# Optimization experiments

Hardware: AMD Instinct MI355X
Metric: run time of the kernel (lower is better)

## Reference

```python
import jax, jax.numpy as jnp
import numpy as np

B_, N, C, NH, NW = 2048, 64, 512, 16, 64  # N == window_size

def setup_inputs() -> dict:
    key = jax.random.key(0)
    k0, k1, k2, k3 = jax.random.split(key, 4)
    std = 0.02
    return {
        "inputs": jax.random.normal(k0, (B_, N, C), jnp.float32),
        "mask": jnp.zeros((NW, N, N), jnp.float32),  # (0 / -inf) additive window mask
        "qkv_w": jax.random.normal(k1, (3 * C, C), jnp.float32) * std,
        "qkv_b": jnp.zeros((3 * C,), jnp.float32),
        "proj_w": jax.random.normal(k2, (C, C), jnp.float32) * std,
        "proj_b": jnp.zeros((C,), jnp.float32),
        "bias_table": jax.random.normal(k3, (2 * N - 1, NH), jnp.float32) * std,
    }

def reference(inputs, mask, qkv_w, qkv_b, proj_w, proj_b, bias_table):
    b, n, c = inputs.shape
    nh = bias_table.shape[1]
    hd = c // nh
    scale = hd ** -0.5
    # qkv projection -> (3, B_, nh, N, hd)
    qkv = (inputs @ qkv_w.T + qkv_b).reshape(b, n, 3, nh, hd).transpose(2, 0, 3, 1, 4)
    q, k, v = qkv[0] * scale, qkv[1], qkv[2]
    attn = jnp.einsum('bhqd,bhkd->bhqk', q, k)  # (B_, nh, N, N)
    # 1D relative position bias, gathered from table
    rel_idx = jnp.arange(n)[:, None] - jnp.arange(n)[None, :] + (n - 1)  # (N, N)
    rel_bias = bias_table[rel_idx]                 # (N, N, nh)
    attn = attn + rel_bias.transpose(2, 0, 1)[None]  # add (nh, N, N)
    # additive window mask
    nw = mask.shape[0]
    attn = attn.reshape(b // nw, nw, nh, n, n) + mask[None, :, None]
    attn = jax.nn.softmax(attn.reshape(b, nh, n, n), axis=-1)
    out = jnp.einsum('bhqk,bhkd->bqhd', attn, v).reshape(b, n, c)
    return out @ proj_w.T + proj_b
```

## Files before the change

### kernel.cpp

```cpp
#include <hip/hip_runtime.h>

typedef __bf16 bf16x8 __attribute__((ext_vector_type(8)));
typedef float f32x4 __attribute__((ext_vector_type(4)));

__device__ __forceinline__ unsigned short f2bf(float x) {
  union { float f; unsigned int u; } c; c.f = x;
  unsigned int r = c.u + 0x7FFFu + ((c.u >> 16) & 1u);
  return (unsigned short)(r >> 16);
}

__global__ __launch_bounds__(256) void f32_to_bf16_vec4(
    const float* __restrict__ in, unsigned short* __restrict__ out, int n4) {
  int i = blockIdx.x * blockDim.x + threadIdx.x;
  int stride = gridDim.x * blockDim.x;
  const float4* in4 = (const float4*)in;
  ushort4* out4 = (ushort4*)out;
  for (; i < n4; i += stride) {
    float4 f = in4[i];
    ushort4 u;
    u.x = f2bf(f.x); u.y = f2bf(f.y); u.z = f2bf(f.z); u.w = f2bf(f.w);
    out4[i] = u;
  }
}

__global__ __launch_bounds__(256) void build_bias_mask(
    const float* __restrict__ bias_table,
    const float* __restrict__ mask,
    float* __restrict__ M) {
  const int idx = blockIdx.x * 256 + threadIdx.x;
  const int k = idx & 63, q = (idx >> 6) & 63, h = (idx >> 12) & 15, w = idx >> 16;
  M[idx] = bias_table[(q - k + 63) * 16 + h] + mask[(w * 64 + q) * 64 + k];
}

#define GLOAD_LDS16(gp, lp)                                                          \
  __builtin_amdgcn_global_load_lds(                                                  \
      (const __attribute__((address_space(1))) unsigned int*)(uintptr_t)(gp),        \
      (__attribute__((address_space(3))) unsigned int*)(uintptr_t)(lp), 16, 0, 0)

template <int NBN, int EPI>
__global__ __launch_bounds__(512, 2) void gemm256(
    const unsigned short* __restrict__ A,
    const unsigned short* __restrict__ B,
    const float* __restrict__ bias,
    void* __restrict__ C0, void* __restrict__ C1, void* __restrict__ C2,
    int ldc) {
  constexpr int K = 512;
  constexpr int NT = K / 64;
  __shared__ __attribute__((aligned(128))) char lds[131072];

  const int t = threadIdx.x;
  const int lane = t & 63;
  const int wid = t >> 6;
  const int wr = wid >> 2, wc = wid & 3;
  const int lr = lane & 15, lg = lane >> 4;

  const int nwg = gridDim.x;
  const int cpx = nwg >> 3;
  const int wgid = (blockIdx.x & 7) * cpx + (blockIdx.x >> 3);
  const int bm = wgid / NBN, bn = wgid % NBN;
  const int m0 = bm * 256, n0 = bn * 256;

  const char* Ab = (const char*)(A + (size_t)m0 * K);
  const char* Bb = (const char*)(B + (size_t)n0 * K);

  const int r3 = t >> 3, ps = t & 7;

  unsigned aoff[2][2], adst[2][2], boff[2][2], bdst[2][2];
#pragma unroll
  for (int j = 0; j < 2; ++j)
#pragma unroll
    for (int i = 0; i < 2; ++i) {
      const int rowA = i * 128 + j * 64 + r3;
      aoff[j][i] = (unsigned)((rowA * K + ((ps ^ (rowA & 7)) << 3)) * 2);
      adst[j][i] = (unsigned)(rowA * 128 + ps * 16);
      const int rowB = i * 128 + ((r3 >> 5) << 6) + j * 32 + (r3 & 31);
      boff[j][i] = (unsigned)((rowB * K + ((ps ^ (rowB & 7)) << 3)) * 2);
      bdst[j][i] = (unsigned)(65536 + rowB * 128 + ps * 16);
    }

#define STAGE_A(j, tt, buf)                                                   \
  do {                                                                        \
    GLOAD_LDS16(Ab + aoff[j][0] + (tt)*128, lds + (buf)*32768 + adst[j][0]);  \
    GLOAD_LDS16(Ab + aoff[j][1] + (tt)*128, lds + (buf)*32768 + adst[j][1]);  \
  } while (0)
#define STAGE_B(j, tt, buf)                                                   \
  do {                                                                        \
    GLOAD_LDS16(Bb + boff[j][0] + (tt)*128, lds + (buf)*32768 + bdst[j][0]);  \
    GLOAD_LDS16(Bb + boff[j][1] + (tt)*128, lds + (buf)*32768 + bdst[j][1]);  \
  } while (0)

  unsigned abase[2], bbase[2];
#pragma unroll
  for (int kk = 0; kk < 2; ++kk) {
    abase[kk] = (unsigned)((wr * 128 + lr) * 128 + (((kk * 4 + lg) ^ (lr & 7)) << 4));
    bbase[kk] = (unsigned)(65536 + (wc * 64 + lr) * 128 + (((kk * 4 + lg) ^ (lr & 7)) << 4));
  }

  f32x4 acc[8][4];
#pragma unroll
  for (int i = 0; i < 8; ++i)
#pragma unroll
    for (int j = 0; j < 4; ++j) acc[i][j] = f32x4{0.f, 0.f, 0.f, 0.f};

#define BAR_IN()                                         \
  __builtin_amdgcn_s_barrier();                          \
  asm volatile("s_waitcnt lgkmcnt(0)" ::: "memory");     \
  __builtin_amdgcn_sched_barrier(0);                     \
  __builtin_amdgcn_s_setprio(1)
#define MFMA16(QM, NTLO)                                                            \
  _Pragma("unroll") for (int mt = 0; mt < 4; ++mt)                                  \
    _Pragma("unroll") for (int nt = 0; nt < 2; ++nt)                                \
      _Pragma("unroll") for (int kk = 0; kk < 2; ++kk)                              \
        acc[(QM)*4 + mt][(NTLO) + nt] = __builtin_amdgcn_mfma_f32_16x16x32_bf16(    \
            af[mt][kk], bfr[(NTLO) + nt][kk], acc[(QM)*4 + mt][(NTLO) + nt], 0, 0, 0)

  STAGE_A(0, 0, 0); STAGE_B(0, 0, 0); STAGE_B(1, 0, 0); STAGE_A(1, 0, 0);
  STAGE_A(0, 1, 1); STAGE_B(0, 1, 1);
  asm volatile("s_waitcnt vmcnt(8)" ::: "memory");
  __builtin_amdgcn_s_barrier();

#pragma unroll
  for (int tt = 0; tt < NT; ++tt) {
    const int buf = tt & 1;
    const int nb = buf ^ 1;
    bf16x8 af[4][2], bfr[4][2];
#pragma unroll
    for (int nt = 0; nt < 2; ++nt)
#pragma unroll
      for (int kk = 0; kk < 2; ++kk)
        bfr[nt][kk] = *(const bf16x8*)(lds + buf * 32768 + bbase[kk] + nt * 2048);
#pragma unroll
    for (int mt = 0; mt < 4; ++mt)
#pragma unroll
      for (int kk = 0; kk < 2; ++kk)
        af[mt][kk] = *(const bf16x8*)(lds + buf * 32768 + abase[kk] + mt * 2048);
    if (tt + 1 < NT) STAGE_B(1, tt + 1, nb);
    BAR_IN();
    MFMA16(0, 0);
    __builtin_amdgcn_s_setprio(0);
    if (tt == NT - 1) asm volatile("s_waitcnt vmcnt(2)" ::: "memory");
    else              asm volatile("s_waitcnt vmcnt(8)" ::: "memory");
    __builtin_amdgcn_s_barrier();
#pragma unroll
    for (int nt = 2; nt < 4; ++nt)
#pragma unroll
      for (int kk = 0; kk < 2; ++kk)
        bfr[nt][kk] = *(const bf16x8*)(lds + buf * 32768 + bbase[kk] + nt * 2048);
    if (tt + 1 < NT) STAGE_A(1, tt + 1, nb);
    BAR_IN();
    MFMA16(0, 2);
    __builtin_amdgcn_s_setprio(0);
    if (tt == NT - 1) asm volatile("s_waitcnt vmcnt(0)" ::: "memory");
    else              asm volatile("s_waitcnt vmcnt(8)" ::: "memory");
    __builtin_amdgcn_s_barrier();
#pragma unroll
    for (int mt = 0; mt < 4; ++mt)
#pragma unroll
      for (int kk = 0; kk < 2; ++kk)
        af[mt][kk] = *(const bf16x8*)(lds + buf * 32768 + abase[kk] + 8192 + mt * 2048);
    if (tt + 2 < NT) STAGE_A(0, tt + 2, buf);
    BAR_IN();
    MFMA16(1, 0);
    __builtin_amdgcn_s_setprio(0);
    if (tt < NT - 1) asm volatile("s_waitcnt vmcnt(8)" ::: "memory");
    __builtin_amdgcn_s_barrier();
    if (tt + 2 < NT) STAGE_B(0, tt + 2, buf);
    BAR_IN();
    MFMA16(1, 2);
    __builtin_amdgcn_s_setprio(0);
    if (tt < NT - 2)       asm volatile("s_waitcnt vmcnt(8)" ::: "memory");
    else if (tt == NT - 2) asm volatile("s_waitcnt vmcnt(4)" ::: "memory");
    __builtin_amdgcn_s_barrier();
  }
#undef MFMA16
#undef BAR_IN
#undef STAGE_A
#undef STAGE_B

#pragma unroll
  for (int qm = 0; qm < 2; ++qm)
#pragma unroll
    for (int mt = 0; mt < 4; ++mt)
#pragma unroll
      for (int nt = 0; nt < 4; ++nt) {
        const int n = n0 + wc * 64 + nt * 16 + lr;
        const float bv = bias[n];
        const f32x4 a4 = acc[qm * 4 + mt][nt];
        if constexpr (EPI == 2) {
          const int part = n >> 9;
          unsigned short* dst = part == 0 ? (unsigned short*)C0
                                 : (part == 1 ? (unsigned short*)C1 : (unsigned short*)C2);
          const float sc = (part == 0) ? 0.17677669529663687f : 1.0f;
          const int hh = (n >> 5) & 15, dd = n & 31;
#pragma unroll
          for (int r = 0; r < 4; ++r) {
            const int m = m0 + wr * 128 + qm * 64 + mt * 16 + lg * 4 + r;
            dst[((size_t)((m >> 6) * 16 + hh) * 64 + (m & 63)) * 32 + dd] =
                f2bf((a4[r] + bv) * sc);
          }
        } else {
#pragma unroll
          for (int r = 0; r < 4; ++r) {
            const int m = m0 + wr * 128 + qm * 64 + mt * 16 + lg * 4 + r;
            ((float*)C0)[(size_t)m * ldc + n] = a4[r] + bv;
          }
        }
      }
}

__global__ __launch_bounds__(128) void attn_kernel(
    const unsigned short* __restrict__ Qh,
    const unsigned short* __restrict__ Kh,
    const unsigned short* __restrict__ Vh,
    const float* __restrict__ M,
    unsigned short* __restrict__ attn_out
) {
  const int wv = threadIdx.x >> 6;
  const int bh = blockIdx.x * 2 + wv;
  const int b = bh >> 4, h = bh & 15;
  const int lane = threadIdx.x & 63;
  const int lr = lane & 15, lg = lane >> 4;

  __shared__ unsigned short VtS[2][32 * 72];
  __shared__ unsigned short PlS[2][16 * 72];
  unsigned short* Vt = VtS[wv];
  unsigned short* Pl = PlS[wv];

  const unsigned short* qb = Qh + (size_t)bh * 2048;
  const unsigned short* kb = Kh + (size_t)bh * 2048;
  const unsigned short* vg = Vh + (size_t)bh * 2048;

  bf16x8 vr[4];
#pragma unroll
  for (int i = 0; i < 4; ++i) vr[i] = ((const bf16x8*)(vg + lane * 32))[i];
  bf16x8 kf[4], qf[4];
#pragma unroll
  for (int nt = 0; nt < 4; ++nt)
    kf[nt] = *(const bf16x8*)(kb + (nt * 16 + lr) * 32 + lg * 8);
#pragma unroll
  for (int mt = 0; mt < 4; ++mt)
    qf[mt] = *(const bf16x8*)(qb + (mt * 16 + lr) * 32 + lg * 8);

  {
    __bf16* vt = (__bf16*)Vt;
#pragma unroll
    for (int d = 0; d < 8; ++d) {
      vt[(d)*72 + lane] = vr[0][d];
      vt[(d + 8) * 72 + lane] = vr[1][d];
      vt[(d + 16) * 72 + lane] = vr[2][d];
      vt[(d + 24) * 72 + lane] = vr[3][d];
    }
  }
  bf16x8 vfrag[2][2];
#pragma unroll
  for (int dt = 0; dt < 2; ++dt)
#pragma unroll
    for (int ki = 0; ki < 2; ++ki)
      vfrag[dt][ki] = *(const bf16x8*)(Vt + (dt * 16 + lr) * 72 + ki * 32 + lg * 8);

  const float* Mb = M + (size_t)((b & 63) * 16 + h) * 4096;

  f32x4 o[4][2];
#pragma unroll
  for (int i = 0; i < 4; ++i)
#pragma unroll
    for (int j = 0; j < 2; ++j) o[i][j] = f32x4{0.f, 0.f, 0.f, 0.f};
  float rinv[4][4];

#pragma unroll
  for (int mt = 0; mt < 4; ++mt) {
    float mv[4][4];
#pragma unroll
    for (int r = 0; r < 4; ++r)
#pragma unroll
      for (int nt = 0; nt < 4; ++nt)
        mv[r][nt] = Mb[(mt * 16 + lg * 4 + r) * 64 + nt * 16 + lr];

    f32x4 s[4];
#pragma unroll
    for (int nt = 0; nt < 4; ++nt) s[nt] = f32x4{0.f, 0.f, 0.f, 0.f};
    __builtin_amdgcn_s_setprio(1);
#pragma unroll
    for (int nt = 0; nt < 4; ++nt)
      s[nt] = __builtin_amdgcn_mfma_f32_16x16x32_bf16(qf[mt], kf[nt], s[nt], 0, 0, 0);
    __builtin_amdgcn_s_setprio(0);

#pragma unroll
    for (int r = 0; r < 4; ++r) {
      float v[4];
#pragma unroll
      for (int nt = 0; nt < 4; ++nt) v[nt] = s[nt][r] + mv[r][nt];
      float mx = fmaxf(fmaxf(v[0], v[1]), fmaxf(v[2], v[3]));
      mx = fmaxf(mx, __shfl_xor(mx, 1, 64));
      mx = fmaxf(mx, __shfl_xor(mx, 2, 64));
      mx = fmaxf(mx, __shfl_xor(mx, 4, 64));
      mx = fmaxf(mx, __shfl_xor(mx, 8, 64));
      float sum = 0.f;
#pragma unroll
      for (int nt = 0; nt < 4; ++nt) {
        v[nt] = __expf(v[nt] - mx);
        sum += v[nt];
      }
      sum += __shfl_xor(sum, 1, 64);
      sum += __shfl_xor(sum, 2, 64);
      sum += __shfl_xor(sum, 4, 64);
      sum += __shfl_xor(sum, 8, 64);
      rinv[mt][r] = __builtin_amdgcn_rcpf(sum);
#pragma unroll
      for (int nt = 0; nt < 4; ++nt)
        Pl[(lg * 4 + r) * 72 + nt * 16 + lr] = f2bf(v[nt]);
    }

    bf16x8 pa[2];
#pragma unroll
    for (int ki = 0; ki < 2; ++ki)
      pa[ki] = *(const bf16x8*)(Pl + lr * 72 + ki * 32 + lg * 8);
    __builtin_amdgcn_s_setprio(1);
#pragma unroll
    for (int dt = 0; dt < 2; ++dt)
#pragma unroll
      for (int ki = 0; ki < 2; ++ki)
        o[mt][dt] = __builtin_amdgcn_mfma_f32_16x16x32_bf16(pa[ki], vfrag[dt][ki], o[mt][dt], 0, 0, 0);
    __builtin_amdgcn_s_setprio(0);
  }

#pragma unroll
  for (int mt = 0; mt < 4; ++mt) {
#pragma unroll
    for (int r = 0; r < 4; ++r) {
      const int m = mt * 16 + lg * 4 + r;
      const float ri = rinv[mt][r];
#pragma unroll
      for (int dt = 0; dt < 2; ++dt) {
        const int d = dt * 16 + lr;
        attn_out[(size_t)(b * 64 + m) * 512 + h * 32 + d] = f2bf(o[mt][dt][r] * ri);
      }
    }
  }
}

extern "C" void kernel_launch(void* const* d_in, const int* in_sizes, int n_in,
                              void* d_out, int out_size, void* d_ws, size_t ws_size,
                              hipStream_t stream) {
  const float* X = (const float*)d_in[0];
  const float* mask = (const float*)d_in[1];
  const float* qkv_w = (const float*)d_in[2];
  const float* qkv_b = (const float*)d_in[3];
  const float* proj_w = (const float*)d_in[4];
  const float* proj_b = (const float*)d_in[5];
  const float* bias_table = (const float*)d_in[6];
  float* out = (float*)d_out;
  char* ws = (char*)d_ws;

  unsigned short* Xb      = (unsigned short*)(ws);
  unsigned short* Qh      = (unsigned short*)(ws + 134217728ull);
  unsigned short* Kh      = (unsigned short*)(ws + 268435456ull);
  unsigned short* Vh      = (unsigned short*)(ws + 402653184ull);
  unsigned short* attnout = (unsigned short*)(ws + 536870912ull);
  unsigned short* qkv_wb  = (unsigned short*)(ws + 671088640ull);
  unsigned short* proj_wb = (unsigned short*)(ws + 672661504ull);
  float*          Mf      = (float*)(ws + 673185792ull);

  f32_to_bf16_vec4<<<2048, 256, 0, stream>>>(X, Xb, 67108864 / 4);
  f32_to_bf16_vec4<<<768, 256, 0, stream>>>(qkv_w, qkv_wb, 786432 / 4);
  f32_to_bf16_vec4<<<256, 256, 0, stream>>>(proj_w, proj_wb, 262144 / 4);
  build_bias_mask<<<16384, 256, 0, stream>>>(bias_table, mask, Mf);

  gemm256<6, 2><<<3072, 512, 0, stream>>>(Xb, qkv_wb, qkv_b, (void*)Qh, (void*)Kh, (void*)Vh, 1536);

  attn_kernel<<<16384, 128, 0, stream>>>(Qh, Kh, Vh, Mf, attnout);

  gemm256<2, 0><<<1024, 512, 0, stream>>>(attnout, proj_wb, proj_b, (void*)out, nullptr, nullptr, 512);
}
```

Baseline: 577.5 us.

## Shrink GEMM tiles to 128x128 with simple double buffering; remap attention blocks

Replaces the 256x256, 8-wave GEMM with a 128x128, 4-wave GEMM that uses a plain double-buffered pipeline: the next K-slice is staged before the current one is computed, with a full vmcnt(0) wait each iteration. This quadruples the number of workgroups and halves LDS per block. The aim is better occupancy and tail balance, at the cost of less operand reuse per tile and a less overlapped schedule. The attention kernel also changes how blocks map to batch and head: each block now holds one head of two windows that are 64 batches apart, which changes how mask and bias rows are shared in cache.

Result: slower. 672.2 us (+16.4%).

```diff
diff --git a/kernel.cpp b/kernel.cpp
--- a/kernel.cpp
+++ b/kernel.cpp
@@ -38,7 +38,7 @@
       (__attribute__((address_space(3))) unsigned int*)(uintptr_t)(lp), 16, 0, 0)
 
 template <int NBN, int EPI>
-__global__ __launch_bounds__(512, 2) void gemm256(
+__global__ __launch_bounds__(256, 2) void gemm128(
     const unsigned short* __restrict__ A,
     const unsigned short* __restrict__ B,
     const float* __restrict__ bias,
@@ -46,166 +46,120 @@
     int ldc) {
   constexpr int K = 512;
   constexpr int NT = K / 64;
-  __shared__ __attribute__((aligned(128))) char lds[131072];
+  __shared__ __attribute__((aligned(128))) char lds[65536];
 
   const int t = threadIdx.x;
   const int lane = t & 63;
   const int wid = t >> 6;
-  const int wr = wid >> 2, wc = wid & 3;
+  const int wr = wid >> 1, wc = wid & 1;
   const int lr = lane & 15, lg = lane >> 4;
 
   const int nwg = gridDim.x;
   const int cpx = nwg >> 3;
   const int wgid = (blockIdx.x & 7) * cpx + (blockIdx.x >> 3);
   const int bm = wgid / NBN, bn = wgid % NBN;
-  const int m0 = bm * 256, n0 = bn * 256;
+  const int m0 = bm * 128, n0 = bn * 128;
 
   const char* Ab = (const char*)(A + (size_t)m0 * K);
   const char* Bb = (const char*)(B + (size_t)n0 * K);
 
   const int r3 = t >> 3, ps = t & 7;
 
-  unsigned aoff[2][2], adst[2][2], boff[2][2], bdst[2][2];
-#pragma unroll
-  for (int j = 0; j < 2; ++j)
-#pragma unroll
-    for (int i = 0; i < 2; ++i) {
-      const int rowA = i * 128 + j * 64 + r3;
-      aoff[j][i] = (unsigned)((rowA * K + ((ps ^ (rowA & 7)) << 3)) * 2);
-      adst[j][i] = (unsigned)(rowA * 128 + ps * 16);
-      const int rowB = i * 128 + ((r3 >> 5) << 6) + j * 32 + (r3 & 31);
-      boff[j][i] = (unsigned)((rowB * K + ((ps ^ (rowB & 7)) << 3)) * 2);
-      bdst[j][i] = (unsigned)(65536 + rowB * 128 + ps * 16);
-    }
-
-#define STAGE_A(j, tt, buf)                                                   \
-  do {                                                                        \
-    GLOAD_LDS16(Ab + aoff[j][0] + (tt)*128, lds + (buf)*32768 + adst[j][0]);  \
-    GLOAD_LDS16(Ab + aoff[j][1] + (tt)*128, lds + (buf)*32768 + adst[j][1]);  \
+  unsigned soff[4], adst[4], bdst[4];
+#pragma unroll
+  for (int i = 0; i < 4; ++i) {
+    const int row = i * 32 + r3;
+    soff[i] = (unsigned)((row * K + ((ps ^ (row & 7)) << 3)) * 2);
+    adst[i] = (unsigned)(row * 128 + ps * 16);
+    bdst[i] = (unsigned)(32768 + row * 128 + ps * 16);
+  }
+
+#define STAGE(tt, buf)                                                          \
+  do {                                                                          \
+    _Pragma("unroll") for (int i = 0; i < 4; ++i)                               \
+      GLOAD_LDS16(Ab + soff[i] + (tt)*128, lds + (buf)*16384 + adst[i]);        \
+    _Pragma("unroll") for (int i = 0; i < 4; ++i)                               \
+      GLOAD_LDS16(Bb + soff[i] + (tt)*128, lds + (buf)*16384 + bdst[i]);        \
   } while (0)
-#define STAGE_B(j, tt, buf)                                                   \
-  do {                                                                        \
-    GLOAD_LDS16(Bb + boff[j][0] + (tt)*128, lds + (buf)*32768 + bdst[j][0]);  \
-    GLOAD_LDS16(Bb + boff[j][1] + (tt)*128, lds + (buf)*32768 + bdst[j][1]);  \
-  } while (0)
 
   unsigned abase[2], bbase[2];
 #pragma unroll
   for (int kk = 0; kk < 2; ++kk) {
-    abase[kk] = (unsigned)((wr * 128 + lr) * 128 + (((kk * 4 + lg) ^ (lr & 7)) << 4));
-    bbase[kk] = (unsigned)(65536 + (wc * 64 + lr) * 128 + (((kk * 4 + lg) ^ (lr & 7)) << 4));
-  }
-
-  f32x4 acc[8][4];
-#pragma unroll
-  for (int i = 0; i < 8; ++i)
+    const unsigned swz = (unsigned)(((kk * 4 + lg) ^ (lr & 7)) << 4);
+    abase[kk] = (unsigned)((wr * 64 + lr) * 128) + swz;
+    bbase[kk] = (unsigned)(32768 + (wc * 64 + lr) * 128) + swz;
+  }
+
+  f32x4 acc[4][4];
+#pragma unroll
+  for (int i = 0; i < 4; ++i)
 #pragma unroll
     for (int j = 0; j < 4; ++j) acc[i][j] = f32x4{0.f, 0.f, 0.f, 0.f};
 
-#define BAR_IN()                                         \
-  __builtin_amdgcn_s_barrier();                          \
-  asm volatile("s_waitcnt lgkmcnt(0)" ::: "memory");     \
-  __builtin_amdgcn_sched_barrier(0);                     \
-  __builtin_amdgcn_s_setprio(1)
-#define MFMA16(QM, NTLO)                                                            \
-  _Pragma("unroll") for (int mt = 0; mt < 4; ++mt)                                  \
-    _Pragma("unroll") for (int nt = 0; nt < 2; ++nt)                                \
-      _Pragma("unroll") for (int kk = 0; kk < 2; ++kk)                              \
-        acc[(QM)*4 + mt][(NTLO) + nt] = __builtin_amdgcn_mfma_f32_16x16x32_bf16(    \
-            af[mt][kk], bfr[(NTLO) + nt][kk], acc[(QM)*4 + mt][(NTLO) + nt], 0, 0, 0)
-
-  STAGE_A(0, 0, 0); STAGE_B(0, 0, 0); STAGE_B(1, 0, 0); STAGE_A(1, 0, 0);
-  STAGE_A(0, 1, 1); STAGE_B(0, 1, 1);
-  asm volatile("s_waitcnt vmcnt(8)" ::: "memory");
+  STAGE(0, 0);
+  asm volatile("s_waitcnt vmcnt(0)" ::: "memory");
   __builtin_amdgcn_s_barrier();
 
 #pragma unroll
   for (int tt = 0; tt < NT; ++tt) {
     const int buf = tt & 1;
     const int nb = buf ^ 1;
+    if (tt + 1 < NT) STAGE(tt + 1, nb);
     bf16x8 af[4][2], bfr[4][2];
 #pragma unroll
-    for (int nt = 0; nt < 2; ++nt)
+    for (int mt = 0; mt < 4; ++mt)
 #pragma unroll
       for (int kk = 0; kk < 2; ++kk)
-        bfr[nt][kk] = *(const bf16x8*)(lds + buf * 32768 + bbase[kk] + nt * 2048);
+        af[mt][kk] = *(const bf16x8*)(lds + buf * 16384 + abase[kk] + mt * 2048);
+#pragma unroll
+    for (int nt = 0; nt < 4; ++nt)
+#pragma unroll
+      for (int kk = 0; kk < 2; ++kk)
+        bfr[nt][kk] = *(const bf16x8*)(lds + buf * 16384 + bbase[kk] + nt * 2048);
+    asm volatile("s_waitcnt lgkmcnt(0)" ::: "memory");
+    __builtin_amdgcn_sched_barrier(0);
+    __builtin_amdgcn_s_setprio(1);
 #pragma unroll
     for (int mt = 0; mt < 4; ++mt)
 #pragma unroll
-      for (int kk = 0; kk < 2; ++kk)
-        af[mt][kk] = *(const bf16x8*)(lds + buf * 32768 + abase[kk] + mt * 2048);
-    if (tt + 1 < NT) STAGE_B(1, tt + 1, nb);
-    BAR_IN();
-    MFMA16(0, 0);
+      for (int nt = 0; nt < 4; ++nt)
+#pragma unroll
+        for (int kk = 0; kk < 2; ++kk)
+          acc[mt][nt] = __builtin_amdgcn_mfma_f32_16x16x32_bf16(
+              af[mt][kk], bfr[nt][kk], acc[mt][nt], 0, 0, 0);
     __builtin_amdgcn_s_setprio(0);
-    if (tt == NT - 1) asm volatile("s_waitcnt vmcnt(2)" ::: "memory");
-    else              asm volatile("s_waitcnt vmcnt(8)" ::: "memory");
+    if (tt + 1 < NT) asm volatile("s_waitcnt vmcnt(0)" ::: "memory");
     __builtin_amdgcn_s_barrier();
-#pragma unroll
-    for (int nt = 2; nt < 4; ++nt)
-#pragma unroll
-      for (int kk = 0; kk < 2; ++kk)
-        bfr[nt][kk] = *(const bf16x8*)(lds + buf * 32768 + bbase[kk] + nt * 2048);
-    if (tt + 1 < NT) STAGE_A(1, tt + 1, nb);
-    BAR_IN();
-    MFMA16(0, 2);
-    __builtin_amdgcn_s_setprio(0);
-    if (tt == NT - 1) asm volatile("s_waitcnt vmcnt(0)" ::: "memory");
-    else              asm volatile("s_waitcnt vmcnt(8)" ::: "memory");
-    __builtin_amdgcn_s_barrier();
-#pragma unroll
-    for (int mt = 0; mt < 4; ++mt)
-#pragma unroll
-      for (int kk = 0; kk < 2; ++kk)
-        af[mt][kk] = *(const bf16x8*)(lds + buf * 32768 + abase[kk] + 8192 + mt * 2048);
-    if (tt + 2 < NT) STAGE_A(0, tt + 2, buf);
-    BAR_IN();
-    MFMA16(1, 0);
-    __builtin_amdgcn_s_setprio(0);
-    if (tt < NT - 1) asm volatile("s_waitcnt vmcnt(8)" ::: "memory");
-    __builtin_amdgcn_s_barrier();
-    if (tt + 2 < NT) STAGE_B(0, tt + 2, buf);
-    BAR_IN();
-    MFMA16(1, 2);
-    __builtin_amdgcn_s_setprio(0);
-    if (tt < NT - 2)       asm volatile("s_waitcnt vmcnt(8)" ::: "memory");
-    else if (tt == NT - 2) asm volatile("s_waitcnt vmcnt(4)" ::: "memory");
-    __builtin_amdgcn_s_barrier();
-  }
-#undef MFMA16
-#undef BAR_IN
-#undef STAGE_A
-#undef STAGE_B
-
-#pragma unroll
-  for (int qm = 0; qm < 2; ++qm)
-#pragma unroll
-    for (int mt = 0; mt < 4; ++mt)
-#pragma unroll
-      for (int nt = 0; nt < 4; ++nt) {
-        const int n = n0 + wc * 64 + nt * 16 + lr;
-        const float bv = bias[n];
-        const f32x4 a4 = acc[qm * 4 + mt][nt];
-        if constexpr (EPI == 2) {
-          const int part = n >> 9;
-          unsigned short* dst = part == 0 ? (unsigned short*)C0
-                                 : (part == 1 ? (unsigned short*)C1 : (unsigned short*)C2);
-          const float sc = (part == 0) ? 0.17677669529663687f : 1.0f;
-          const int hh = (n >> 5) & 15, dd = n & 31;
-#pragma unroll
-          for (int r = 0; r < 4; ++r) {
-            const int m = m0 + wr * 128 + qm * 64 + mt * 16 + lg * 4 + r;
-            dst[((size_t)((m >> 6) * 16 + hh) * 64 + (m & 63)) * 32 + dd] =
-                f2bf((a4[r] + bv) * sc);
-          }
-        } else {
-#pragma unroll
-          for (int r = 0; r < 4; ++r) {
-            const int m = m0 + wr * 128 + qm * 64 + mt * 16 + lg * 4 + r;
-            ((float*)C0)[(size_t)m * ldc + n] = a4[r] + bv;
-          }
+  }
+#undef STAGE
+
+#pragma unroll
+  for (int mt = 0; mt < 4; ++mt)
+#pragma unroll
+    for (int nt = 0; nt < 4; ++nt) {
+      const int n = n0 + wc * 64 + nt * 16 + lr;
+      const float bv = bias[n];
+      const f32x4 a4 = acc[mt][nt];
+      if constexpr (EPI == 2) {
+        const int part = n >> 9;
+        unsigned short* dst = part == 0 ? (unsigned short*)C0
+                               : (part == 1 ? (unsigned short*)C1 : (unsigned short*)C2);
+        const float sc = (part == 0) ? 0.17677669529663687f : 1.0f;
+        const int hh = (n >> 5) & 15, dd = n & 31;
+#pragma unroll
+        for (int r = 0; r < 4; ++r) {
+          const int m = m0 + wr * 64 + mt * 16 + lg * 4 + r;
+          dst[((size_t)((m >> 6) * 16 + hh) * 64 + (m & 63)) * 32 + dd] =
+              f2bf((a4[r] + bv) * sc);
+        }
+      } else {
+#pragma unroll
+        for (int r = 0; r < 4; ++r) {
+          const int m = m0 + wr * 64 + mt * 16 + lg * 4 + r;
+          ((float*)C0)[(size_t)m * ldc + n] = a4[r] + bv;
         }
       }
+    }
 }
 
 __global__ __launch_bounds__(128) void attn_kernel(
@@ -216,8 +170,11 @@
     unsigned short* __restrict__ attn_out
 ) {
   const int wv = threadIdx.x >> 6;
-  const int bh = blockIdx.x * 2 + wv;
-  const int b = bh >> 4, h = bh & 15;
+  const int idx = blockIdx.x;
+  const int h = idx & 15;
+  const int g = idx >> 4;
+  const int b = (g & 63) + ((g >> 6) << 7) + (wv << 6);
+  const int bh = b * 16 + h;
   const int lane = threadIdx.x & 63;
   const int lr = lane & 15, lg = lane >> 4;
 
@@ -366,9 +323,9 @@
   f32_to_bf16_vec4<<<256, 256, 0, stream>>>(proj_w, proj_wb, 262144 / 4);
   build_bias_mask<<<16384, 256, 0, stream>>>(bias_table, mask, Mf);
 
-  gemm256<6, 2><<<3072, 512, 0, stream>>>(Xb, qkv_wb, qkv_b, (void*)Qh, (void*)Kh, (void*)Vh, 1536);
+  gemm128<12, 2><<<12288, 256, 0, stream>>>(Xb, qkv_wb, qkv_b, (void*)Qh, (void*)Kh, (void*)Vh, 1536);
 
   attn_kernel<<<16384, 128, 0, stream>>>(Qh, Kh, Vh, Mf, attnout);
 
-  gemm256<2, 0><<<1024, 512, 0, stream>>>(attnout, proj_wb, proj_b, (void*)out, nullptr, nullptr, 512);
-}
+  gemm128<4, 0><<<4096, 256, 0, stream>>>(attnout, proj_wb, proj_b, (void*)out, nullptr, nullptr, 512);
+}
```
